# Performance work log

Measured on AMD Instinct MI355X. Metric: run time of the kernel, lower is better.

The kernel has to match this reference:

```python
import jax, jax.numpy as jnp
import numpy as np

# Module hyperparameters (match init_kwargs)
N_IN, N_OUT = 1024, 256
B = 512
T_MAX, DT = 100.0, 1.0
TAU_SYN, TAU_MEM, TAU_SOFT = 5.0, 10.0, 0.5
N_STEPS = int(round(T_MAX / DT))  # 100


def _conn_mask():
    # sequential even partition of inputs across output branches
    m = np.zeros((N_OUT, N_IN), np.float32)
    base, rem = N_IN // N_OUT, N_IN % N_OUT
    cur = 0
    for o in range(N_OUT):
        s = base + (1 if o < rem else 0)
        m[o, cur:cur + s] = 1.0
        cur += s
    return jnp.asarray(m)

CONN = _conn_mask()  # [n_out, n_in]


def setup_inputs() -> dict:
    key = jax.random.key(0)
    k1, k2 = jax.random.split(key)
    spike_times_in = jax.random.uniform(k1, (B, N_IN), jnp.float32) * T_MAX
    W = 1.0 + 0.1 * jax.random.normal(k2, (N_OUT, N_IN), jnp.float32)
    return {"spike_times_in": spike_times_in, "W": W}


def reference(spike_times_in, W):
    # spike_times_in: [B, n_in]; W: [n_out, n_in]
    times = jnp.arange(N_STEPS, dtype=jnp.float32) * DT            # [T]
    # PSP kernel exp(-(t - s)/tau_syn) * [t >= s], per input and timestep
    dtm = times[None, None, :] - spike_times_in[:, :, None]        # [B, n_in, T]
    psp = jnp.where(dtm >= 0, jnp.exp(-dtm / TAU_SYN), 0.0)        # [B, n_in, T]
    # Input current per branch per step: one big GEMM instead of T small ones
    I = jnp.einsum('bit,oi->tbo', psp, W * CONN)                   # [T, B, n_out]
    # Leaky-integrator recurrence v_t = v_{t-1} + (-v_{t-1} + I_t) * dt/tau_mem
    a = DT / TAU_MEM
    def step(v, I_t):
        v = v + (-v + I_t) * a
        return v, v
    v0 = jnp.zeros((spike_times_in.shape[0], N_OUT), jnp.float32)
    _, v_trace = jax.lax.scan(step, v0, I)                         # [T, B, n_out]
    v_trace = jnp.moveaxis(v_trace, 0, -1)                         # [B, n_out, T]
    # soft-argmax readout over time
    w = jax.nn.softmax(v_trace / TAU_SOFT, axis=-1)
    spike_times_out = jnp.sum(w * times, axis=-1)                  # [B, n_out]
    return spike_times_out
```

## Files before the change

### kernel.cpp

```cpp
#include <hip/hip_runtime.h>
#include <math.h>


#define N_IN   1024
#define N_OUT  256
#define BATCH  512
#define NSTEPS 100

__global__ __launch_bounds__(N_OUT) void dendritic_kernel(
    const float* __restrict__ spikes,
    const float* __restrict__ W,
    float* __restrict__ out)
{
    const int b = blockIdx.x;
    const int o = threadIdx.x;

    const float4 s4 = *reinterpret_cast<const float4*>(spikes + b * N_IN + o * 4);
    const float4 w4 = *reinterpret_cast<const float4*>(W + o * N_IN + o * 4);

    const float A0 = w4.x * __expf(0.2f * s4.x);
    const float A1 = w4.y * __expf(0.2f * s4.y);
    const float A2 = w4.z * __expf(0.2f * s4.z);
    const float A3 = w4.w * __expf(0.2f * s4.w);

    float v = 0.f;
    float den0 = 0.f, den1 = 0.f;
    float num0 = 0.f, num1 = 0.f;

#pragma unroll
    for (int t = 0; t < NSTEPS; ++t) {
        const float tf = (float)t;
        const float E  = 0.1f * __builtin_expf(-0.2f * tf);
        float S = (s4.x <= tf ? A0 : 0.f)
                + (s4.y <= tf ? A1 : 0.f)
                + (s4.z <= tf ? A2 : 0.f)
                + (s4.w <= tf ? A3 : 0.f);
        v = fmaf(0.9f, v, E * S);
        const float e = __expf(2.0f * v);
        if (t & 1) { den1 += e; num1 = fmaf(e, tf, num1); }
        else       { den0 += e; num0 = fmaf(e, tf, num0); }
    }

    out[b * N_OUT + o] = (num0 + num1) / (den0 + den1);
}

extern "C" void kernel_launch(void* const* d_in, const int* in_sizes, int n_in,
                              void* d_out, int out_size, void* d_ws, size_t ws_size,
                              hipStream_t stream) {
    const float* spikes = (const float*)d_in[0];
    const float* W      = (const float*)d_in[1];
    float* out          = (float*)d_out;

    dendritic_kernel<<<BATCH, N_OUT, 0, stream>>>(spikes, W, out);
}
```

Measured before the change: 61.53 us.

## Split time recurrence into parallel chunks with closed-form chunk carry-in

Splits the 100-step leaky-integrator recurrence into four 25-step chunks, each run by a separate thread. Each chunk's starting membrane value comes from a closed-form geometric-series sum of the earlier chunks' contributions, combined through shared memory. Partial softmax numerators and denominators are then reduced across chunks. This shortens the serial dependency chain per thread and raises thread-level parallelism, at the cost of extra exp work, two block syncs, and possible floating-point drift from the closed-form carry.

```diff
diff --git a/kernel.cpp b/kernel.cpp
--- a/kernel.cpp
+++ b/kernel.cpp
@@ -5,43 +5,100 @@
 #define N_IN   1024
 #define N_OUT  256
 #define BATCH  512
-#define NSTEPS 100
+#define NCHUNK 4
+#define CLEN   25
+#define OTILE  128
+#define TPB    (NCHUNK * OTILE)
 
-__global__ __launch_bounds__(N_OUT) void dendritic_kernel(
+#if __has_builtin(__builtin_amdgcn_exp2f)
+#define EXP2(x) __builtin_amdgcn_exp2f(x)
+#else
+#define EXP2(x) __expf(0.69314718056f * (x))
+#endif
+
+__global__ __launch_bounds__(TPB, 8) void dendritic_kernel(
     const float* __restrict__ spikes,
     const float* __restrict__ W,
     float* __restrict__ out)
 {
-    const int b = blockIdx.x;
-    const int o = threadIdx.x;
+    const int b     = blockIdx.x >> 1;
+    const int obase = (blockIdx.x & 1) * OTILE;
+    const int tid   = threadIdx.x;
+    const int ol    = tid & (OTILE - 1);
+    const int c     = tid >> 7;
+    const int o     = obase + ol;
+    const float t0f = (float)(CLEN * c);
 
     const float4 s4 = *reinterpret_cast<const float4*>(spikes + b * N_IN + o * 4);
     const float4 w4 = *reinterpret_cast<const float4*>(W + o * N_IN + o * 4);
 
-    const float A0 = w4.x * __expf(0.2f * s4.x);
-    const float A1 = w4.y * __expf(0.2f * s4.y);
-    const float A2 = w4.z * __expf(0.2f * s4.z);
-    const float A3 = w4.w * __expf(0.2f * s4.w);
+    const float KB    = 2.0f * 1.44269504089f * 0.1f;
+    const float L2E5  = 0.2f * 1.44269504089f;
+    const float LOG2R = L2E5 + __builtin_log2f(0.9f);
+    const float C1    = __builtin_expf(-4.8f) /
+                        (0.9f * __builtin_expf(0.2f) - 1.0f);
+    const float G1    = __builtin_expf(25.0f * __builtin_logf(0.9f));
 
-    float v = 0.f;
-    float den0 = 0.f, den1 = 0.f;
-    float num0 = 0.f, num1 = 0.f;
+    const float U0 = (c == 0) ? KB
+                   : (c == 1) ? KB * __builtin_expf(-5.0f)
+                   : (c == 2) ? KB * __builtin_expf(-10.0f)
+                   :            KB * __builtin_expf(-15.0f);
 
+    const float a0 = (w4.x * U0) * EXP2(L2E5 * s4.x);
+    const float a1 = (w4.y * U0) * EXP2(L2E5 * s4.y);
+    const float a2 = (w4.z * U0) * EXP2(L2E5 * s4.z);
+    const float a3 = (w4.w * U0) * EXP2(L2E5 * s4.w);
+
+    const float sh0 = s4.x - t0f, sh1 = s4.y - t0f,
+                sh2 = s4.z - t0f, sh3 = s4.w - t0f;
+
+    const float n0 = fminf(25.0f, fmaxf(0.0f, 25.0f - __builtin_ceilf(sh0)));
+    const float n1 = fminf(25.0f, fmaxf(0.0f, 25.0f - __builtin_ceilf(sh1)));
+    const float n2 = fminf(25.0f, fmaxf(0.0f, 25.0f - __builtin_ceilf(sh2)));
+    const float n3 = fminf(25.0f, fmaxf(0.0f, 25.0f - __builtin_ceilf(sh3)));
+    const float zend = C1 * (a0 * (EXP2(LOG2R * n0) - 1.0f) +
+                             a1 * (EXP2(LOG2R * n1) - 1.0f) +
+                             a2 * (EXP2(LOG2R * n2) - 1.0f) +
+                             a3 * (EXP2(LOG2R * n3) - 1.0f));
+
+    __shared__ float zl[NCHUNK][OTILE];
+    zl[c][ol] = zend;
+    __syncthreads();
+
+    float v = 0.0f;
+    if (c == 1)      v = zl[0][ol];
+    else if (c == 2) v = fmaf(G1, zl[0][ol], zl[1][ol]);
+    else if (c == 3) v = fmaf(G1, fmaf(G1, zl[0][ol], zl[1][ol]), zl[2][ol]);
+
+    float den0 = 0.f, den1 = 0.f, den2 = 0.f, den3 = 0.f;
+    float num0 = 0.f, num1 = 0.f, num2 = 0.f, num3 = 0.f;
 #pragma unroll
-    for (int t = 0; t < NSTEPS; ++t) {
-        const float tf = (float)t;
-        const float E  = 0.1f * __builtin_expf(-0.2f * tf);
-        float S = (s4.x <= tf ? A0 : 0.f)
-                + (s4.y <= tf ? A1 : 0.f)
-                + (s4.z <= tf ? A2 : 0.f)
-                + (s4.w <= tf ? A3 : 0.f);
-        v = fmaf(0.9f, v, E * S);
-        const float e = __expf(2.0f * v);
-        if (t & 1) { den1 += e; num1 = fmaf(e, tf, num1); }
-        else       { den0 += e; num0 = fmaf(e, tf, num0); }
+    for (int k = 0; k < CLEN; ++k) {
+        const float kf = (float)k;
+        const float uk = __builtin_expf(-0.2f * kf);
+        float S = (sh0 <= kf ? a0 : 0.f) + (sh1 <= kf ? a1 : 0.f)
+                + (sh2 <= kf ? a2 : 0.f) + (sh3 <= kf ? a3 : 0.f);
+        v = fmaf(0.9f, v, uk * S);
+        const float e = EXP2(v);
+        if      ((k & 3) == 0) { den0 += e; num0 = fmaf(e, kf, num0); }
+        else if ((k & 3) == 1) { den1 += e; num1 = fmaf(e, kf, num1); }
+        else if ((k & 3) == 2) { den2 += e; num2 = fmaf(e, kf, num2); }
+        else                   { den3 += e; num3 = fmaf(e, kf, num3); }
     }
 
-    out[b * N_OUT + o] = (num0 + num1) / (den0 + den1);
+    const float den = (den0 + den1) + (den2 + den3);
+    const float num = fmaf(t0f, den, (num0 + num1) + (num2 + num3));
+
+    __shared__ float2 red[NCHUNK][OTILE];
+    red[c][ol] = make_float2(num, den);
+    __syncthreads();
+
+    if (c == 0) {
+        const float2 r0 = red[0][ol], r1 = red[1][ol],
+                     r2 = red[2][ol], r3 = red[3][ol];
+        out[b * N_OUT + o] = ((r0.x + r1.x) + (r2.x + r3.x)) /
+                             ((r0.y + r1.y) + (r2.y + r3.y));
+    }
 }
 
 extern "C" void kernel_launch(void* const* d_in, const int* in_sizes, int n_in,
@@ -51,5 +108,5 @@
     const float* W      = (const float*)d_in[1];
     float* out          = (float*)d_out;
 
-    dendritic_kernel<<<BATCH, N_OUT, 0, stream>>>(spikes, W, out);
+    dendritic_kernel<<<BATCH * 2, TPB, 0, stream>>>(spikes, W, out);
 }
```

Measured after the change: 60.93 us. Within noise of the previous version (-1.0%).
